# Optimization experiments

Hardware: AMD Instinct MI355X
Metric: run time of the kernel (lower is better)

## Reference

```python
import jax, jax.numpy as jnp
import numpy as np

SCALE = 10  # scaling_factor
ETA = 1.0   # init arg eta
EPS = 1e-20


def setup_inputs() -> dict:
    key = jax.random.key(0)
    k1, k2, k3 = jax.random.split(key, 3)
    B, H, W = 32, 1280, 1280
    h, w = H // SCALE, W // SCALE
    output = jax.random.uniform(k1, (B, 1, H, W), dtype=jnp.float32)
    target = jax.random.uniform(k2, (B, 1, H, W), dtype=jnp.float32)
    inp = jax.random.uniform(k3, (B, 1, h, w), dtype=jnp.float32)
    return {"output": output, "target": target, "inp": inp}


def _box_downsample(x):
    # scipy valid convolve2d with ones(10,10)/100 then [::10,::10] strided slice
    # == non-overlapping 10x10 average pooling (H, W divisible by 10).
    B, H, W = x.shape
    return x.reshape(B, H // SCALE, SCALE, W // SCALE, SCALE).mean(axis=(2, 4))


def reference(output, target, inp):
    # MSE term: conv output is computed from detached numpy in the original,
    # so no gradient flows through the pooling path -> stop_gradient.
    pooled = jax.lax.stop_gradient(_box_downsample(output[:, 0]))  # [B, h, w]
    mse = jnp.mean(ETA * (inp[:, 0] - pooled) ** 2)
    # BCE-style term with exact-zero replacement (matches x[x==0]=1e-20)
    om = jnp.where(output == 0, EPS, output)
    oc_raw = 1.0 - output
    oc = jnp.where(oc_raw == 0, EPS, oc_raw)
    bce = -jnp.mean(target * jnp.log(om) + (1.0 - target) * jnp.log(oc))
    loss = mse + bce
    return jnp.full((1, 1), loss)  # original returns a (1,1) tensor
```

## Files before the change

kernel.cpp:

```cpp
#include <hip/hip_runtime.h>


#define BATCH 32
#define HH 1280
#define WW 1280
#define PH 128
#define PW 128
#define SC 10
#define NT 320
#define KD 10
#define PD 4

static constexpr float EPSV = 1e-20f;
static constexpr float LN2  = 0.6931471805599453f;
static constexpr float INV_NB = 1.0f / (float)(BATCH * HH * WW);
static constexpr float INV_NM = 1.0f / (float)(BATCH * PH * PW);

__global__ __launch_bounds__(NT, 8) void srloss_kernel(
    const float* __restrict__ output,
    const float* __restrict__ target,
    const float* __restrict__ inp,
    float* __restrict__ out)
{
    __shared__ float psum[PW];
    __shared__ float red[NT / 64];

    const int t = threadIdx.x;
    const int band = blockIdx.x;
    const int b = band >> 7;
    const int pr = band & 127;

    if (t < PW) psum[t] = 0.0f;
    __syncthreads();

    const size_t base = ((size_t)b * HH + (size_t)pr * SC) * WW;
    const float4* __restrict__ o4p = (const float4*)(output + base) + t;
    const float4* __restrict__ t4p = (const float4*)(target + base) + t;

    float4 ob[PD], tb[PD];
    #pragma unroll
    for (int k = 0; k < PD; ++k) {
        ob[k] = o4p[NT * k];
        tb[k] = t4p[NT * k];
    }

    float acc2 = 0.0f;
    float accd = 0.0f;
    float s0 = 0.0f, s1 = 0.0f;
    #pragma unroll
    for (int k = 0; k < KD; ++k) {
        const float4 o4 = ob[k & (PD - 1)];
        const float4 t4 = tb[k & (PD - 1)];
        if (k + PD < KD) {
            ob[k & (PD - 1)] = o4p[NT * (k + PD)];
            tb[k & (PD - 1)] = t4p[NT * (k + PD)];
        }
        const float o[4]  = {o4.x, o4.y, o4.z, o4.w};
        const float tg[4] = {t4.x, t4.y, t4.z, t4.w};
        #pragma unroll
        for (int j = 0; j < 4; ++j) {
            const float om = fmaxf(o[j], EPSV);
            const float oc = fmaxf(1.0f - o[j], EPSV);
            const float l1 = __log2f(om);
            const float l2 = __log2f(oc);
            acc2 += l2;
            accd += tg[j] * (l1 - l2);
        }
        s0 += o[0] + o[1];
        s1 += o[2] + o[3];
    }
    const float bce_acc = LN2 * (acc2 + accd);

    const int col0 = 4 * t;
    const int p0 = col0 / SC;
    if ((col0 % SC) == 8) {
        atomicAdd(&psum[p0],     s0);
        atomicAdd(&psum[p0 + 1], s1);
    } else {
        atomicAdd(&psum[p0], s0 + s1);
    }
    __syncthreads();

    float mse_acc = 0.0f;
    if (t < PW) {
        const float pooled = psum[t] * (1.0f / (float)(SC * SC));
        const float iv = inp[(size_t)band * PW + t];
        const float d = iv - pooled;
        mse_acc = d * d;
    }

    float contrib = (-INV_NB) * bce_acc + INV_NM * mse_acc;

    #pragma unroll
    for (int off = 32; off > 0; off >>= 1)
        contrib += __shfl_down(contrib, off, 64);
    if ((t & 63) == 0) red[t >> 6] = contrib;
    __syncthreads();
    if (t == 0) {
        float s = 0.0f;
        #pragma unroll
        for (int w = 0; w < NT / 64; ++w) s += red[w];
        atomicAdd(out, s);
    }
}

extern "C" void kernel_launch(void* const* d_in, const int* in_sizes, int n_in,
                              void* d_out, int out_size, void* d_ws, size_t ws_size,
                              hipStream_t stream) {
    const float* output = (const float*)d_in[0];
    const float* target = (const float*)d_in[1];
    const float* inp    = (const float*)d_in[2];
    float* out = (float*)d_out;

    hipMemsetAsync(out, 0, sizeof(float), stream);

    srloss_kernel<<<BATCH * PH, NT, 0, stream>>>(output, target, inp, out);
}
```

Baseline: 436.9 us.

## Shrink block to 128 threads with 25 float4 loads per thread

Cuts the block from 320 threads to 128, so each thread handles 25 float4 pairs across the 10-row band instead of 10. Because the column phase now rotates with a period of 5, the pooled partial sums go into five per-phase accumulators that are remapped to pooled columns before the shared atomics. The explicit software prefetch ring is dropped in favour of fully unrolled direct loads that the compiler can schedule. The goal is more memory-level parallelism per thread and fewer shared atomics and idle threads in the MSE stage, at the cost of more registers and fewer waves per block.

```diff
diff --git a/kernel.cpp b/kernel.cpp
--- a/kernel.cpp
+++ b/kernel.cpp
@@ -7,9 +7,9 @@
 #define PH 128
 #define PW 128
 #define SC 10
-#define NT 320
-#define KD 10
-#define PD 4
+#define NT 128
+#define KD 25
+#define NPH 5
 
 static constexpr float EPSV = 1e-20f;
 static constexpr float LN2  = 0.6931471805599453f;
@@ -30,31 +30,22 @@
     const int b = band >> 7;
     const int pr = band & 127;
 
-    if (t < PW) psum[t] = 0.0f;
+    psum[t] = 0.0f;
     __syncthreads();
 
     const size_t base = ((size_t)b * HH + (size_t)pr * SC) * WW;
     const float4* __restrict__ o4p = (const float4*)(output + base) + t;
     const float4* __restrict__ t4p = (const float4*)(target + base) + t;
 
-    float4 ob[PD], tb[PD];
-    #pragma unroll
-    for (int k = 0; k < PD; ++k) {
-        ob[k] = o4p[NT * k];
-        tb[k] = t4p[NT * k];
-    }
-
     float acc2 = 0.0f;
     float accd = 0.0f;
-    float s0 = 0.0f, s1 = 0.0f;
+    float s0[NPH] = {0, 0, 0, 0, 0};
+    float s1[NPH] = {0, 0, 0, 0, 0};
     #pragma unroll
     for (int k = 0; k < KD; ++k) {
-        const float4 o4 = ob[k & (PD - 1)];
-        const float4 t4 = tb[k & (PD - 1)];
-        if (k + PD < KD) {
-            ob[k & (PD - 1)] = o4p[NT * (k + PD)];
-            tb[k & (PD - 1)] = t4p[NT * (k + PD)];
-        }
+        const int p = k % NPH;
+        const float4 o4 = o4p[NT * k];
+        const float4 t4 = t4p[NT * k];
         const float o[4]  = {o4.x, o4.y, o4.z, o4.w};
         const float tg[4] = {t4.x, t4.y, t4.z, t4.w};
         #pragma unroll
@@ -66,28 +57,30 @@
             acc2 += l2;
             accd += tg[j] * (l1 - l2);
         }
-        s0 += o[0] + o[1];
-        s1 += o[2] + o[3];
+        s0[p] += o[0] + o[1];
+        s1[p] += o[2] + o[3];
     }
     const float bce_acc = LN2 * (acc2 + accd);
 
-    const int col0 = 4 * t;
-    const int p0 = col0 / SC;
-    if ((col0 % SC) == 8) {
-        atomicAdd(&psum[p0],     s0);
-        atomicAdd(&psum[p0 + 1], s1);
-    } else {
-        atomicAdd(&psum[p0], s0 + s1);
+    #pragma unroll
+    for (int p = 0; p < NPH; ++p) {
+        int r = t + NT * p;
+        if (r >= 320) r -= 320;
+        const int col0 = 4 * r;
+        const int p0 = col0 / SC;
+        if ((col0 % SC) == 8) {
+            atomicAdd(&psum[p0],     s0[p]);
+            atomicAdd(&psum[p0 + 1], s1[p]);
+        } else {
+            atomicAdd(&psum[p0], s0[p] + s1[p]);
+        }
     }
     __syncthreads();
 
-    float mse_acc = 0.0f;
-    if (t < PW) {
-        const float pooled = psum[t] * (1.0f / (float)(SC * SC));
-        const float iv = inp[(size_t)band * PW + t];
-        const float d = iv - pooled;
-        mse_acc = d * d;
-    }
+    const float pooled = psum[t] * (1.0f / (float)(SC * SC));
+    const float iv = inp[(size_t)band * PW + t];
+    const float d = iv - pooled;
+    const float mse_acc = d * d;
 
     float contrib = (-INV_NB) * bce_acc + INV_NM * mse_acc;
 
@@ -97,10 +90,7 @@
     if ((t & 63) == 0) red[t >> 6] = contrib;
     __syncthreads();
     if (t == 0) {
-        float s = 0.0f;
-        #pragma unroll
-        for (int w = 0; w < NT / 64; ++w) s += red[w];
-        atomicAdd(out, s);
+        atomicAdd(out, red[0] + red[1]);
     }
 }
 
```

After: 540.0 us. 23.6% more time.
